# Kernel tuning notes

Measured on AMD Instinct MI355X. Metric: run time of the kernel, lower is better.

## Reference

```python
import jax, jax.numpy as jnp
import numpy as np

NV = 20000; NC = 20000; E = 500000
IN_SHAPE = 2; PE_DIM = 8; HID = 64; NL = 3
EPS = 1e-7  # GENConv message eps


def _lin(x, w, b):
    return x @ w + b


def _encode(x, pe, ew, eb, pw1, pb1, pw2, pb2):
    # relu(cat([Linear(x), 0.5*(pe_mlp(pe)+pe_mlp(-pe))], dim=1))
    def pe_mlp(p):
        return _lin(jax.nn.relu(_lin(p, pw1, pb1)), pw2, pb2)
    h = jnp.concatenate([_lin(x, ew, eb), 0.5 * (pe_mlp(pe) + pe_mlp(-pe))], axis=1)
    return jax.nn.relu(h)


def _genconv(x_src, x_dst, src, dst, ewt, lew, leb, w1, b1, w2, b2, n_dst):
    # GENConv(aggr='softmax', t=1, norm=None, msg_norm=False, edge_dim=1)
    msg = jax.nn.relu(x_src[src] + _lin(ewt, lew, leb)) + EPS  # [E, HID]
    m = jax.ops.segment_max(msg, dst, num_segments=n_dst)      # stable segment softmax
    ex = jnp.exp(msg - m[dst])
    s = jax.ops.segment_sum(ex, dst, num_segments=n_dst)
    agg = jax.ops.segment_sum(ex / (s[dst] + 1e-16) * msg, dst, num_segments=n_dst)
    out = agg + x_dst
    return _lin(jax.nn.relu(_lin(out, w1, b1)), w2, b2)  # MLP [hid -> 2hid -> hid]


def setup_inputs() -> dict:
    key = jax.random.key(0)
    ks = iter(jax.random.split(key, 64))
    d = {}
    d['x_vals'] = jax.random.normal(next(ks), (NV, IN_SHAPE), jnp.float32)
    d['x_cons'] = jax.random.normal(next(ks), (NC, IN_SHAPE), jnp.float32)
    d['pe_vals'] = jax.random.normal(next(ks), (NV, PE_DIM), jnp.float32)
    d['pe_cons'] = jax.random.normal(next(ks), (NC, PE_DIM), jnp.float32)
    d['edge_index_v2c'] = jnp.stack([
        jax.random.randint(next(ks), (E,), 0, NV),
        jax.random.randint(next(ks), (E,), 0, NC)])
    d['edge_index_c2v'] = jnp.stack([
        jax.random.randint(next(ks), (E,), 0, NC),
        jax.random.randint(next(ks), (E,), 0, NV)])
    d['edge_weight_v2c'] = jax.random.normal(next(ks), (E, 1), jnp.float32)
    d['edge_weight_c2v'] = jax.random.normal(next(ks), (E, 1), jnp.float32)
    def p(shape):
        return jax.random.normal(next(ks), shape, jnp.float32) * 0.05
    for k_ in ['vals', 'cons']:
        d[f'enc_{k_}_w'] = p((IN_SHAPE, HID // 2)); d[f'enc_{k_}_b'] = p((HID // 2,))
        d[f'pe_{k_}_w1'] = p((PE_DIM, HID)); d[f'pe_{k_}_b1'] = p((HID,))
        d[f'pe_{k_}_w2'] = p((HID, HID // 2)); d[f'pe_{k_}_b2'] = p((HID // 2,))
    for c in ['v2c', 'c2v']:
        d[f'{c}_edge_w'] = p((NL, 1, HID)); d[f'{c}_edge_b'] = p((NL, HID))
        d[f'{c}_w1'] = p((NL, HID, 2 * HID)); d[f'{c}_b1'] = p((NL, 2 * HID))
        d[f'{c}_w2'] = p((NL, 2 * HID, HID)); d[f'{c}_b2'] = p((NL, HID))
    for k_ in ['vals', 'cons']:
        d[f'pred_{k_}_w1'] = p((HID, HID)); d[f'pred_{k_}_b1'] = p((HID,))
        d[f'pred_{k_}_w2'] = p((HID, 1)); d[f'pred_{k_}_b2'] = p((1,))
    return d


def reference(x_vals, x_cons, pe_vals, pe_cons, edge_index_v2c, edge_index_c2v,
              edge_weight_v2c, edge_weight_c2v,
              enc_vals_w, enc_vals_b, pe_vals_w1, pe_vals_b1, pe_vals_w2, pe_vals_b2,
              enc_cons_w, enc_cons_b, pe_cons_w1, pe_cons_b1, pe_cons_w2, pe_cons_b2,
              v2c_edge_w, v2c_edge_b, v2c_w1, v2c_b1, v2c_w2, v2c_b2,
              c2v_edge_w, c2v_edge_b, c2v_w1, c2v_b1, c2v_w2, c2v_b2,
              pred_vals_w1, pred_vals_b1, pred_vals_w2, pred_vals_b2,
              pred_cons_w1, pred_cons_b1, pred_cons_w2, pred_cons_b2):
    vals = _encode(x_vals, pe_vals, enc_vals_w, enc_vals_b,
                   pe_vals_w1, pe_vals_b1, pe_vals_w2, pe_vals_b2)
    cons = _encode(x_cons, pe_cons, enc_cons_w, enc_cons_b,
                   pe_cons_w1, pe_cons_b1, pe_cons_w2, pe_cons_b2)
    hv, hc = [], []
    for i in range(NL):
        cons = _genconv(vals, cons, edge_index_v2c[0], edge_index_v2c[1],
                        edge_weight_v2c, v2c_edge_w[i], v2c_edge_b[i],
                        v2c_w1[i], v2c_b1[i], v2c_w2[i], v2c_b2[i], NC)
        vals = _genconv(cons, vals, edge_index_c2v[0], edge_index_c2v[1],
                        edge_weight_c2v, c2v_edge_w[i], c2v_edge_b[i],
                        c2v_w1[i], c2v_b1[i], c2v_w2[i], c2v_b2[i], NV)
        hc.append(cons); hv.append(vals)
    V = jnp.stack(hv)  # [NL, NV, HID]
    C = jnp.stack(hc)  # [NL, NC, HID]
    pv = _lin(jax.nn.relu(_lin(V, pred_vals_w1, pred_vals_b1)), pred_vals_w2, pred_vals_b2)
    pc = _lin(jax.nn.relu(_lin(C, pred_cons_w1, pred_cons_b1)), pred_cons_w2, pred_cons_b2)
    return pv[..., 0].T, pc[..., 0].T  # [NV, NL], [NC, NL]
```

## Files before the change

### kernel.cpp

```cpp
#include <hip/hip_runtime.h>

#define NVN 20000
#define NCN 20000
#define NE  500000
#define HID 64
#define NLAYER 3
#define TN 40
#define BSH 8
#define NB 79
#define P1E 2048

__device__ __forceinline__ float relu_(float x) { return fmaxf(x, 0.0f); }

__global__ __launch_bounds__(256) void binhist_kernel(
    const int* __restrict__ dstA, const int* __restrict__ dstB,
    int* __restrict__ binszA, int* __restrict__ binszB)
{
    __shared__ int cA[NB], cB[NB];
    int t = threadIdx.x;
    int e0 = blockIdx.x * P1E;
    if (t < NB) { cA[t] = 0; cB[t] = 0; }
    __syncthreads();
    for (int i = t; i < P1E; i += 256) {
        int e = e0 + i;
        if (e < NE) {
            atomicAdd(&cA[dstA[e] >> BSH], 1);
            atomicAdd(&cB[dstB[e] >> BSH], 1);
        }
    }
    __syncthreads();
    if (t < NB) {
        if (cA[t] > 0) atomicAdd(&binszA[t], cA[t]);
        if (cB[t] > 0) atomicAdd(&binszB[t], cB[t]);
    }
}

__global__ __launch_bounds__(256) void binscan_kernel(
    const int* __restrict__ binszA, int* __restrict__ binbaseA, int* __restrict__ bincurA,
    const int* __restrict__ binszB, int* __restrict__ binbaseB, int* __restrict__ bincurB)
{
    const int* binsz = blockIdx.x ? binszB : binszA;
    int* binbase     = blockIdx.x ? binbaseB : binbaseA;
    int* bincur      = blockIdx.x ? bincurB : bincurA;
    __shared__ int p[256];
    int t = threadIdx.x;
    p[t] = (t < NB) ? binsz[t] : 0;
    __syncthreads();
    for (int off = 1; off < 256; off <<= 1) {
        int v = (t >= off) ? p[t - off] : 0;
        __syncthreads();
        p[t] += v;
        __syncthreads();
    }
    if (t < NB) { int b = (t == 0) ? 0 : p[t - 1]; binbase[t] = b; bincur[t] = b; }
    if (t == NB) binbase[NB] = p[NB - 1];
}

__global__ __launch_bounds__(256) void scatter_p1_kernel(
    const int* __restrict__ eiA, const float* __restrict__ ewA,
    int* __restrict__ bincurA, int2* __restrict__ stageA,
    const int* __restrict__ eiB, const float* __restrict__ ewB,
    int* __restrict__ bincurB, int2* __restrict__ stageB)
{
    __shared__ int rnk[P1E];
    __shared__ int cnt[NB], base_[NB];
    int t = threadIdx.x;
    int e0 = blockIdx.x * P1E;

    for (int g = 0; g < 2; ++g) {
        const int* ei   = g ? eiB : eiA;
        const float* ew = g ? ewB : ewA;
        int* bincur     = g ? bincurB : bincurA;
        int2* stage     = g ? stageB : stageA;

        if (t < NB) cnt[t] = 0;
        __syncthreads();
        for (int i = t; i < P1E; i += 256) {
            int e = e0 + i;
            if (e < NE) {
                int d = ei[NE + e];
                rnk[i] = atomicAdd(&cnt[d >> BSH], 1);
            }
        }
        __syncthreads();
        if (t < NB && cnt[t] > 0) base_[t] = atomicAdd(&bincur[t], cnt[t]);
        __syncthreads();
        for (int i = t; i < P1E; i += 256) {
            int e = e0 + i;
            if (e < NE) {
                int s = ei[e], d = ei[NE + e];
                float w = ew[e];
                stage[base_[d >> BSH] + rnk[i]] =
                    make_int2((int)((unsigned)s | ((unsigned)d << 16)), __float_as_int(w));
            }
        }
        __syncthreads();
    }
}

__global__ __launch_bounds__(1024) void scatter_p2_kernel(
    const int* __restrict__ binbaseA, const int2* __restrict__ stageA,
    int* __restrict__ rowptrA, int2* __restrict__ pairA,
    const int* __restrict__ binbaseB, const int2* __restrict__ stageB,
    int* __restrict__ rowptrB, int2* __restrict__ pairB)
{
    __shared__ int deg[256], pfx[256], cur[256];
    int g = blockIdx.x / NB;
    int b = blockIdx.x % NB;
    const int* binbase = g ? binbaseB : binbaseA;
    const int2* stage  = g ? stageB : stageA;
    int* rowptr        = g ? rowptrB : rowptrA;
    int2* pair         = g ? pairB : pairA;

    int d0 = b << BSH;
    int d1 = min(d0 + 256, NCN);
    int nd = d1 - d0;
    int t = threadIdx.x;
    int estart = binbase[b], eend = binbase[b + 1];

    if (t < 256) deg[t] = 0;
    __syncthreads();
    for (int e = estart + t; e < eend; e += 1024) {
        int dst = (int)((unsigned)stage[e].x >> 16);
        atomicAdd(&deg[dst - d0], 1);
    }
    __syncthreads();
    if (t < 256) pfx[t] = deg[t];
    __syncthreads();
    for (int off = 1; off < 256; off <<= 1) {
        int v = (t >= off && t < 256) ? pfx[t - off] : 0;
        __syncthreads();
        if (t < 256) pfx[t] += v;
        __syncthreads();
    }
    if (t < nd) {
        int ex = estart + pfx[t] - deg[t];
        rowptr[d0 + t] = ex;
        cur[t] = ex;
    }
    if (t == 0) rowptr[d1] = eend;
    __syncthreads();
    for (int e = estart + t; e < eend; e += 1024) {
        int2 s = stage[e];
        unsigned u = (unsigned)s.x;
        int src = (int)(u & 0xFFFFu);
        int dst = (int)(u >> 16);
        int p = atomicAdd(&cur[dst - d0], 1);
        pair[p] = make_int2(src, s.y);
    }
}

__global__ __launch_bounds__(256) void encode2_kernel(
    const float* __restrict__ xv, const float* __restrict__ pev,
    const float* __restrict__ ewv, const float* __restrict__ ebv,
    const float* __restrict__ pw1v, const float* __restrict__ pb1v,
    const float* __restrict__ pw2v, const float* __restrict__ pb2v,
    const float* __restrict__ xc, const float* __restrict__ pec,
    const float* __restrict__ ewc, const float* __restrict__ ebc,
    const float* __restrict__ pw1c, const float* __restrict__ pb1c,
    const float* __restrict__ pw2c, const float* __restrict__ pb2c,
    float* __restrict__ outv, float* __restrict__ outc)
{
    __shared__ float sh[4][64];
    const int VB = (NVN + 3) / 4;
    int wave = threadIdx.x >> 6, lane = threadIdx.x & 63;
    int b = blockIdx.x;
    bool isC = (b >= VB);
    const float* x   = isC ? xc : xv;
    const float* pe  = isC ? pec : pev;
    const float* ew  = isC ? ewc : ewv;
    const float* eb  = isC ? ebc : ebv;
    const float* pw1 = isC ? pw1c : pw1v;
    const float* pb1 = isC ? pb1c : pb1v;
    const float* pw2 = isC ? pw2c : pw2v;
    const float* pb2 = isC ? pb2c : pb2v;
    float* out = isC ? outc : outv;
    int N = isC ? NCN : NVN;
    int n = (isC ? b - VB : b) * 4 + wave;
    if (n >= N) return;

    float accp = pb1[lane], accm = accp;
#pragma unroll
    for (int k = 0; k < 8; ++k) {
        float p = pe[n * 8 + k];
        float w = pw1[k * 64 + lane];
        accp += p * w;
        accm -= p * w;
    }
    float hs = 0.5f * (relu_(accp) + relu_(accm));
    float* my = sh[wave];
    my[lane] = hs;
    __builtin_amdgcn_wave_barrier();

    int col = lane & 31;
    float peo = pb2[col];
#pragma unroll
    for (int k = 0; k < 64; k += 4) {
        float4 hv = *(const float4*)(my + k);
        peo = fmaf(hv.x, pw2[(k + 0) * 32 + col], peo);
        peo = fmaf(hv.y, pw2[(k + 1) * 32 + col], peo);
        peo = fmaf(hv.z, pw2[(k + 2) * 32 + col], peo);
        peo = fmaf(hv.w, pw2[(k + 3) * 32 + col], peo);
    }
    float lino = x[n * 2 + 0] * ew[col] + x[n * 2 + 1] * ew[32 + col] + eb[col];
    float h = (lane < 32) ? lino : peo;
    out[n * 64 + lane] = relu_(h);
}

__global__ __launch_bounds__(256) void edge_agg_kernel(
    const float* __restrict__ xsrc,
    const float* __restrict__ xdst,
    const int* __restrict__ rowptr,
    const int2* __restrict__ pair,
    const float* __restrict__ lew,
    const float* __restrict__ leb,
    float* __restrict__ oa,
    int N)
{
    int wave = threadIdx.x >> 6, lane = threadIdx.x & 63;
    int n = blockIdx.x * 4 + wave;
    if (n >= N) return;

    int start = __builtin_amdgcn_readfirstlane(rowptr[n]);
    int end   = __builtin_amdgcn_readfirstlane(rowptr[n + 1]);
    float lw = lew[lane], lb = leb[lane];
    float xd = xdst[n * 64 + lane];

    float den = 0.0f, num = 0.0f;
    int j = start;

    if (j + 16 <= end) {
        int2 pb[16];
#pragma unroll
        for (int c = 0; c < 16; ++c) pb[c] = pair[j + c];

        for (; j + 32 <= end; j += 16) {
            float xv[16];
#pragma unroll
            for (int c = 0; c < 16; ++c) xv[c] = xsrc[pb[c].x * 64 + lane];
            int2 pn[16];
#pragma unroll
            for (int c = 0; c < 16; ++c) pn[c] = pair[j + 16 + c];
#pragma unroll
            for (int c = 0; c < 16; ++c) {
                float msg = relu_(fmaf(__int_as_float(pb[c].y), lw, xv[c] + lb)) + 1e-7f;
                float e = __expf(msg);
                den += e;
                num = fmaf(e, msg, num);
            }
#pragma unroll
            for (int c = 0; c < 16; ++c) pb[c] = pn[c];
        }
        {
            float xv[16];
#pragma unroll
            for (int c = 0; c < 16; ++c) xv[c] = xsrc[pb[c].x * 64 + lane];
#pragma unroll
            for (int c = 0; c < 16; ++c) {
                float msg = relu_(fmaf(__int_as_float(pb[c].y), lw, xv[c] + lb)) + 1e-7f;
                float e = __expf(msg);
                den += e;
                num = fmaf(e, msg, num);
            }
            j += 16;
        }
    }
    for (; j + 8 <= end; j += 8) {
        int2 p8[8];
#pragma unroll
        for (int c = 0; c < 8; ++c) p8[c] = pair[j + c];
        float xv[8];
#pragma unroll
        for (int c = 0; c < 8; ++c) xv[c] = xsrc[p8[c].x * 64 + lane];
#pragma unroll
        for (int c = 0; c < 8; ++c) {
            float msg = relu_(fmaf(__int_as_float(p8[c].y), lw, xv[c] + lb)) + 1e-7f;
            float e = __expf(msg);
            den += e;
            num = fmaf(e, msg, num);
        }
    }
    for (; j < end; ++j) {
        int2 p = pair[j];
        float xv = xsrc[p.x * 64 + lane];
        float msg = relu_(fmaf(__int_as_float(p.y), lw, xv + lb)) + 1e-7f;
        float e = __expf(msg);
        den += e;
        num = fmaf(e, msg, num);
    }

    oa[n * 64 + lane] = num / (den + 1e-16f) + xd;
}

__global__ __launch_bounds__(256, 4) void mlp_kernel(
    const float* __restrict__ oa,
    float* __restrict__ feat,
    const float* __restrict__ w1,
    const float* __restrict__ b1,
    const float* __restrict__ w2,
    const float* __restrict__ b2,
    const float* __restrict__ pw1,
    const float* __restrict__ pb1,
    const float* __restrict__ pw2,
    const float* __restrict__ pb2,
    float* __restrict__ outp,
    int N, int layer)
{
    __shared__ float act[TN][68];
    __shared__ float hid[TN][132];
    __shared__ float b1s[128];
    __shared__ float b2s[64];
    __shared__ float pb1s[64];
    __shared__ float pw2s[64];

    int tid = threadIdx.x;
    if (tid < 128) b1s[tid] = b1[tid];
    if (tid < 64) { b2s[tid] = b2[tid]; pb1s[tid] = pb1[tid]; pw2s[tid] = pw2[tid]; }
    float pb2v = pb2[0];

    int o4 = (tid & 31) * 4;
    int o2 = (tid & 31) * 2;
    int n5 = (tid >> 5) * 5;
    __syncthreads();

    int ntiles = N / TN;
    for (int tile = blockIdx.x; tile < ntiles; tile += gridDim.x) {
        int base = tile * TN;
        {
            const float4* g4 = (const float4*)(oa + (size_t)base * 64);
            for (int i = tid; i < TN * 16; i += 256)
                *(float4*)&act[i >> 4][(i & 15) * 4] = g4[i];
        }
        __syncthreads();

        {
            float acc[5][4];
#pragma unroll
            for (int i = 0; i < 5; ++i)
#pragma unroll
                for (int q = 0; q < 4; ++q) acc[i][q] = b1s[o4 + q];
#pragma unroll 2
            for (int k = 0; k < 64; k += 4) {
                float4 a[5];
#pragma unroll
                for (int i = 0; i < 5; ++i) a[i] = *(const float4*)&act[n5 + i][k];
                float4 w0 = *(const float4*)&w1[(k + 0) * 128 + o4];
                float4 wq1 = *(const float4*)&w1[(k + 1) * 128 + o4];
                float4 wq2 = *(const float4*)&w1[(k + 2) * 128 + o4];
                float4 wq3 = *(const float4*)&w1[(k + 3) * 128 + o4];
#pragma unroll
                for (int i = 0; i < 5; ++i) {
                    acc[i][0] = fmaf(a[i].x, w0.x, acc[i][0]);
                    acc[i][1] = fmaf(a[i].x, w0.y, acc[i][1]);
                    acc[i][2] = fmaf(a[i].x, w0.z, acc[i][2]);
                    acc[i][3] = fmaf(a[i].x, w0.w, acc[i][3]);
                    acc[i][0] = fmaf(a[i].y, wq1.x, acc[i][0]);
                    acc[i][1] = fmaf(a[i].y, wq1.y, acc[i][1]);
                    acc[i][2] = fmaf(a[i].y, wq1.z, acc[i][2]);
                    acc[i][3] = fmaf(a[i].y, wq1.w, acc[i][3]);
                    acc[i][0] = fmaf(a[i].z, wq2.x, acc[i][0]);
                    acc[i][1] = fmaf(a[i].z, wq2.y, acc[i][1]);
                    acc[i][2] = fmaf(a[i].z, wq2.z, acc[i][2]);
                    acc[i][3] = fmaf(a[i].z, wq2.w, acc[i][3]);
                    acc[i][0] = fmaf(a[i].w, wq3.x, acc[i][0]);
                    acc[i][1] = fmaf(a[i].w, wq3.y, acc[i][1]);
                    acc[i][2] = fmaf(a[i].w, wq3.z, acc[i][2]);
                    acc[i][3] = fmaf(a[i].w, wq3.w, acc[i][3]);
                }
            }
#pragma unroll
            for (int i = 0; i < 5; ++i) {
                float4 h4 = make_float4(relu_(acc[i][0]), relu_(acc[i][1]),
                                        relu_(acc[i][2]), relu_(acc[i][3]));
                *(float4*)&hid[n5 + i][o4] = h4;
            }
        }
        __syncthreads();

        {
            float acc[5][2];
#pragma unroll
            for (int i = 0; i < 5; ++i) { acc[i][0] = b2s[o2]; acc[i][1] = b2s[o2 + 1]; }
#pragma unroll 2
            for (int k = 0; k < 128; k += 4) {
                float4 a[5];
#pragma unroll
                for (int i = 0; i < 5; ++i) a[i] = *(const float4*)&hid[n5 + i][k];
                float2 w0 = *(const float2*)&w2[(k + 0) * 64 + o2];
                float2 wq1 = *(const float2*)&w2[(k + 1) * 64 + o2];
                float2 wq2 = *(const float2*)&w2[(k + 2) * 64 + o2];
                float2 wq3 = *(const float2*)&w2[(k + 3) * 64 + o2];
#pragma unroll
                for (int i = 0; i < 5; ++i) {
                    acc[i][0] = fmaf(a[i].x, w0.x, acc[i][0]);
                    acc[i][1] = fmaf(a[i].x, w0.y, acc[i][1]);
                    acc[i][0] = fmaf(a[i].y, wq1.x, acc[i][0]);
                    acc[i][1] = fmaf(a[i].y, wq1.y, acc[i][1]);
                    acc[i][0] = fmaf(a[i].z, wq2.x, acc[i][0]);
                    acc[i][1] = fmaf(a[i].z, wq2.y, acc[i][1]);
                    acc[i][0] = fmaf(a[i].w, wq3.x, acc[i][0]);
                    acc[i][1] = fmaf(a[i].w, wq3.y, acc[i][1]);
                }
            }
#pragma unroll
            for (int i = 0; i < 5; ++i) {
                float2 r2 = make_float2(acc[i][0], acc[i][1]);
                *(float2*)&feat[(size_t)(base + n5 + i) * 64 + o2] = r2;
                *(float2*)&act[n5 + i][o2] = r2;
            }
        }
        __syncthreads();

        {
            float acc[5][2];
#pragma unroll
            for (int i = 0; i < 5; ++i) { acc[i][0] = pb1s[o2]; acc[i][1] = pb1s[o2 + 1]; }
#pragma unroll 2
            for (int k = 0; k < 64; k += 4) {
                float4 a[5];
#pragma unroll
                for (int i = 0; i < 5; ++i) a[i] = *(const float4*)&act[n5 + i][k];
                float2 w0 = *(const float2*)&pw1[(k + 0) * 64 + o2];
                float2 wq1 = *(const float2*)&pw1[(k + 1) * 64 + o2];
                float2 wq2 = *(const float2*)&pw1[(k + 2) * 64 + o2];
                float2 wq3 = *(const float2*)&pw1[(k + 3) * 64 + o2];
#pragma unroll
                for (int i = 0; i < 5; ++i) {
                    acc[i][0] = fmaf(a[i].x, w0.x, acc[i][0]);
                    acc[i][1] = fmaf(a[i].x, w0.y, acc[i][1]);
                    acc[i][0] = fmaf(a[i].y, wq1.x, acc[i][0]);
                    acc[i][1] = fmaf(a[i].y, wq1.y, acc[i][1]);
                    acc[i][0] = fmaf(a[i].z, wq2.x, acc[i][0]);
                    acc[i][1] = fmaf(a[i].z, wq2.y, acc[i][1]);
                    acc[i][0] = fmaf(a[i].w, wq3.x, acc[i][0]);
                    acc[i][1] = fmaf(a[i].w, wq3.y, acc[i][1]);
                }
            }
            float pw2a = pw2s[o2], pw2b = pw2s[o2 + 1];
            float ps[5];
#pragma unroll
            for (int i = 0; i < 5; ++i)
                ps[i] = relu_(acc[i][0]) * pw2a + relu_(acc[i][1]) * pw2b;
#pragma unroll
            for (int msk = 16; msk >= 1; msk >>= 1) {
#pragma unroll
                for (int i = 0; i < 5; ++i)
                    ps[i] += __shfl_xor(ps[i], msk, 64);
            }
            if ((tid & 31) == 0) {
#pragma unroll
                for (int i = 0; i < 5; ++i)
                    outp[(size_t)(base + n5 + i) * NLAYER + layer] = ps[i] + pb2v;
            }
        }
        __syncthreads();
    }
}

extern "C" void kernel_launch(void* const* d_in, const int* in_sizes, int n_in,
                              void* d_out, int out_size, void* d_ws, size_t ws_size,
                              hipStream_t stream)
{
    const float* x_vals   = (const float*)d_in[0];
    const float* x_cons   = (const float*)d_in[1];
    const float* pe_vals  = (const float*)d_in[2];
    const float* pe_cons  = (const float*)d_in[3];
    const int*   ei_v2c   = (const int*)d_in[4];
    const int*   ei_c2v   = (const int*)d_in[5];
    const float* ew_v2c   = (const float*)d_in[6];
    const float* ew_c2v   = (const float*)d_in[7];
    const float* enc_vals_w = (const float*)d_in[8];
    const float* enc_vals_b = (const float*)d_in[9];
    const float* pe_vals_w1 = (const float*)d_in[10];
    const float* pe_vals_b1 = (const float*)d_in[11];
    const float* pe_vals_w2 = (const float*)d_in[12];
    const float* pe_vals_b2 = (const float*)d_in[13];
    const float* enc_cons_w = (const float*)d_in[14];
    const float* enc_cons_b = (const float*)d_in[15];
    const float* pe_cons_w1 = (const float*)d_in[16];
    const float* pe_cons_b1 = (const float*)d_in[17];
    const float* pe_cons_w2 = (const float*)d_in[18];
    const float* pe_cons_b2 = (const float*)d_in[19];
    const float* v2c_edge_w = (const float*)d_in[20];
    const float* v2c_edge_b = (const float*)d_in[21];
    const float* v2c_w1     = (const float*)d_in[22];
    const float* v2c_b1     = (const float*)d_in[23];
    const float* v2c_w2     = (const float*)d_in[24];
    const float* v2c_b2     = (const float*)d_in[25];
    const float* c2v_edge_w = (const float*)d_in[26];
    const float* c2v_edge_b = (const float*)d_in[27];
    const float* c2v_w1     = (const float*)d_in[28];
    const float* c2v_b1     = (const float*)d_in[29];
    const float* c2v_w2     = (const float*)d_in[30];
    const float* c2v_b2     = (const float*)d_in[31];
    const float* pred_vals_w1 = (const float*)d_in[32];
    const float* pred_vals_b1 = (const float*)d_in[33];
    const float* pred_vals_w2 = (const float*)d_in[34];
    const float* pred_vals_b2 = (const float*)d_in[35];
    const float* pred_cons_w1 = (const float*)d_in[36];
    const float* pred_cons_b1 = (const float*)d_in[37];
    const float* pred_cons_w2 = (const float*)d_in[38];
    const float* pred_cons_b2 = (const float*)d_in[39];

    float* out = (float*)d_out;
    float* out_c = out + (size_t)NVN * NLAYER;

    const size_t NF = (size_t)NVN * 64;

    float* ws     = (float*)d_ws;
    float* feat_v = ws;
    float* feat_c = feat_v + NF;
    float* oa     = feat_c + NF;
    int2* v2c_pair  = (int2*)(oa + NF);
    int2* c2v_pair  = v2c_pair + NE;
    int2* v2c_stage = c2v_pair + NE;
    int2* c2v_stage = v2c_stage + NE;
    int* ip = (int*)(c2v_stage + NE);
    int* v2c_binsz   = ip; ip += NB;
    int* c2v_binsz   = ip; ip += NB;
    int* v2c_binbase = ip; ip += NB + 1;
    int* c2v_binbase = ip; ip += NB + 1;
    int* v2c_bincur  = ip; ip += NB;
    int* c2v_bincur  = ip; ip += NB;
    int* v2c_rowptr  = ip; ip += NCN + 1;
    int* c2v_rowptr  = ip; ip += NVN + 1;

    const int p1b = (NE + P1E - 1) / P1E;

    hipMemsetAsync(v2c_binsz, 0, (size_t)(2 * NB) * sizeof(int), stream);
    binhist_kernel<<<p1b, 256, 0, stream>>>(ei_v2c + NE, ei_c2v + NE,
                                            v2c_binsz, c2v_binsz);
    binscan_kernel<<<2, 256, 0, stream>>>(v2c_binsz, v2c_binbase, v2c_bincur,
                                          c2v_binsz, c2v_binbase, c2v_bincur);
    scatter_p1_kernel<<<p1b, 256, 0, stream>>>(
        ei_v2c, ew_v2c, v2c_bincur, v2c_stage,
        ei_c2v, ew_c2v, c2v_bincur, c2v_stage);
    scatter_p2_kernel<<<2 * NB, 1024, 0, stream>>>(
        v2c_binbase, v2c_stage, v2c_rowptr, v2c_pair,
        c2v_binbase, c2v_stage, c2v_rowptr, c2v_pair);

    encode2_kernel<<<(NVN + 3) / 4 + (NCN + 3) / 4, 256, 0, stream>>>(
        x_vals, pe_vals, enc_vals_w, enc_vals_b,
        pe_vals_w1, pe_vals_b1, pe_vals_w2, pe_vals_b2,
        x_cons, pe_cons, enc_cons_w, enc_cons_b,
        pe_cons_w1, pe_cons_b1, pe_cons_w2, pe_cons_b2,
        feat_v, feat_c);

    for (int i = 0; i < NLAYER; ++i) {
        edge_agg_kernel<<<(NCN + 3) / 4, 256, 0, stream>>>(
            feat_v, feat_c, v2c_rowptr, v2c_pair,
            v2c_edge_w + (size_t)i * HID, v2c_edge_b + (size_t)i * HID,
            oa, NCN);
        mlp_kernel<<<500, 256, 0, stream>>>(
            oa, feat_c,
            v2c_w1 + (size_t)i * 8192, v2c_b1 + (size_t)i * 128,
            v2c_w2 + (size_t)i * 8192, v2c_b2 + (size_t)i * 64,
            pred_cons_w1, pred_cons_b1, pred_cons_w2, pred_cons_b2,
            out_c, NCN, i);
        edge_agg_kernel<<<(NVN + 3) / 4, 256, 0, stream>>>(
            feat_c, feat_v, c2v_rowptr, c2v_pair,
            c2v_edge_w + (size_t)i * HID, c2v_edge_b + (size_t)i * HID,
            oa, NVN);
        mlp_kernel<<<500, 256, 0, stream>>>(
            oa, feat_v,
            c2v_w1 + (size_t)i * 8192, c2v_b1 + (size_t)i * 128,
            c2v_w2 + (size_t)i * 8192, c2v_b2 + (size_t)i * 64,
            pred_vals_w1, pred_vals_b1, pred_vals_w2, pred_vals_b2,
            out, NVN, i);
    }
}
```

Baseline: 435.3 us.

## Fuse softmax edge aggregation into the per-tile MLP kernel

Merges the per-node softmax aggregation kernel into the MLP kernel. Each wave aggregates 10 destination rows directly into the shared activation tile, so the intermediate aggregate buffer is no longer written to and read back from global memory. This also halves the kernel launches per layer. The cost is parallelism for the gather phase: only NV/40 blocks of 256 threads run, each wave walking its rows one after another, so far fewer waves are available to hide the latency of the random gathers.

```diff
diff --git a/kernel.cpp b/kernel.cpp
--- a/kernel.cpp
+++ b/kernel.cpp
@@ -207,93 +207,13 @@
     out[n * 64 + lane] = relu_(h);
 }
 
-__global__ __launch_bounds__(256) void edge_agg_kernel(
+__global__ __launch_bounds__(256) void agg_mlp_kernel(
     const float* __restrict__ xsrc,
     const float* __restrict__ xdst,
     const int* __restrict__ rowptr,
     const int2* __restrict__ pair,
     const float* __restrict__ lew,
     const float* __restrict__ leb,
-    float* __restrict__ oa,
-    int N)
-{
-    int wave = threadIdx.x >> 6, lane = threadIdx.x & 63;
-    int n = blockIdx.x * 4 + wave;
-    if (n >= N) return;
-
-    int start = __builtin_amdgcn_readfirstlane(rowptr[n]);
-    int end   = __builtin_amdgcn_readfirstlane(rowptr[n + 1]);
-    float lw = lew[lane], lb = leb[lane];
-    float xd = xdst[n * 64 + lane];
-
-    float den = 0.0f, num = 0.0f;
-    int j = start;
-
-    if (j + 16 <= end) {
-        int2 pb[16];
-#pragma unroll
-        for (int c = 0; c < 16; ++c) pb[c] = pair[j + c];
-
-        for (; j + 32 <= end; j += 16) {
-            float xv[16];
-#pragma unroll
-            for (int c = 0; c < 16; ++c) xv[c] = xsrc[pb[c].x * 64 + lane];
-            int2 pn[16];
-#pragma unroll
-            for (int c = 0; c < 16; ++c) pn[c] = pair[j + 16 + c];
-#pragma unroll
-            for (int c = 0; c < 16; ++c) {
-                float msg = relu_(fmaf(__int_as_float(pb[c].y), lw, xv[c] + lb)) + 1e-7f;
-                float e = __expf(msg);
-                den += e;
-                num = fmaf(e, msg, num);
-            }
-#pragma unroll
-            for (int c = 0; c < 16; ++c) pb[c] = pn[c];
-        }
-        {
-            float xv[16];
-#pragma unroll
-            for (int c = 0; c < 16; ++c) xv[c] = xsrc[pb[c].x * 64 + lane];
-#pragma unroll
-            for (int c = 0; c < 16; ++c) {
-                float msg = relu_(fmaf(__int_as_float(pb[c].y), lw, xv[c] + lb)) + 1e-7f;
-                float e = __expf(msg);
-                den += e;
-                num = fmaf(e, msg, num);
-            }
-            j += 16;
-        }
-    }
-    for (; j + 8 <= end; j += 8) {
-        int2 p8[8];
-#pragma unroll
-        for (int c = 0; c < 8; ++c) p8[c] = pair[j + c];
-        float xv[8];
-#pragma unroll
-        for (int c = 0; c < 8; ++c) xv[c] = xsrc[p8[c].x * 64 + lane];
-#pragma unroll
-        for (int c = 0; c < 8; ++c) {
-            float msg = relu_(fmaf(__int_as_float(p8[c].y), lw, xv[c] + lb)) + 1e-7f;
-            float e = __expf(msg);
-            den += e;
-            num = fmaf(e, msg, num);
-        }
-    }
-    for (; j < end; ++j) {
-        int2 p = pair[j];
-        float xv = xsrc[p.x * 64 + lane];
-        float msg = relu_(fmaf(__int_as_float(p.y), lw, xv + lb)) + 1e-7f;
-        float e = __expf(msg);
-        den += e;
-        num = fmaf(e, msg, num);
-    }
-
-    oa[n * 64 + lane] = num / (den + 1e-16f) + xd;
-}
-
-__global__ __launch_bounds__(256, 4) void mlp_kernel(
-    const float* __restrict__ oa,
     float* __restrict__ feat,
     const float* __restrict__ w1,
     const float* __restrict__ b1,
@@ -314,22 +234,91 @@
     __shared__ float pw2s[64];
 
     int tid = threadIdx.x;
+    int wave = tid >> 6, lane = tid & 63;
     if (tid < 128) b1s[tid] = b1[tid];
     if (tid < 64) { b2s[tid] = b2[tid]; pb1s[tid] = pb1[tid]; pw2s[tid] = pw2[tid]; }
     float pb2v = pb2[0];
+    float lw = lew[lane], lb = leb[lane];
 
     int o4 = (tid & 31) * 4;
     int o2 = (tid & 31) * 2;
     int n5 = (tid >> 5) * 5;
-    __syncthreads();
 
     int ntiles = N / TN;
     for (int tile = blockIdx.x; tile < ntiles; tile += gridDim.x) {
         int base = tile * TN;
-        {
-            const float4* g4 = (const float4*)(oa + (size_t)base * 64);
-            for (int i = tid; i < TN * 16; i += 256)
-                *(float4*)&act[i >> 4][(i & 15) * 4] = g4[i];
+
+        for (int q = 0; q < TN / 4; ++q) {
+            int row = wave * (TN / 4) + q;
+            int n = base + row;
+            int start = __builtin_amdgcn_readfirstlane(rowptr[n]);
+            int end   = __builtin_amdgcn_readfirstlane(rowptr[n + 1]);
+            float xd = xdst[(size_t)n * 64 + lane];
+
+            float den = 0.0f, num = 0.0f;
+            int j = start;
+
+            if (j + 16 <= end) {
+                int2 pb[16];
+#pragma unroll
+                for (int c = 0; c < 16; ++c) pb[c] = pair[j + c];
+
+                for (; j + 32 <= end; j += 16) {
+                    float xv[16];
+#pragma unroll
+                    for (int c = 0; c < 16; ++c) xv[c] = xsrc[pb[c].x * 64 + lane];
+                    int2 pn[16];
+#pragma unroll
+                    for (int c = 0; c < 16; ++c) pn[c] = pair[j + 16 + c];
+#pragma unroll
+                    for (int c = 0; c < 16; ++c) {
+                        float msg = relu_(fmaf(__int_as_float(pb[c].y), lw, xv[c] + lb)) + 1e-7f;
+                        float e = __expf(msg);
+                        den += e;
+                        num = fmaf(e, msg, num);
+                    }
+#pragma unroll
+                    for (int c = 0; c < 16; ++c) pb[c] = pn[c];
+                }
+                {
+                    float xv[16];
+#pragma unroll
+                    for (int c = 0; c < 16; ++c) xv[c] = xsrc[pb[c].x * 64 + lane];
+#pragma unroll
+                    for (int c = 0; c < 16; ++c) {
+                        float msg = relu_(fmaf(__int_as_float(pb[c].y), lw, xv[c] + lb)) + 1e-7f;
+                        float e = __expf(msg);
+                        den += e;
+                        num = fmaf(e, msg, num);
+                    }
+                    j += 16;
+                }
+            }
+            for (; j + 8 <= end; j += 8) {
+                int2 p8[8];
+#pragma unroll
+                for (int c = 0; c < 8; ++c) p8[c] = pair[j + c];
+                float xv[8];
+#pragma unroll
+                for (int c = 0; c < 8; ++c) xv[c] = xsrc[p8[c].x * 64 + lane];
+#pragma unroll
+                for (int c = 0; c < 8; ++c) {
+                    float msg = relu_(fmaf(__int_as_float(p8[c].y), lw, xv[c] + lb)) + 1e-7f;
+                    float e = __expf(msg);
+                    den += e;
+                    num = fmaf(e, msg, num);
+                }
+            }
+            for (; j < end; ++j) {
+                int2 p = pair[j];
+                float xv = xsrc[p.x * 64 + lane];
+                float msg = relu_(fmaf(__int_as_float(p.y), lw, xv + lb)) + 1e-7f;
+                float e = __expf(msg);
+                den += e;
+                num = fmaf(e, msg, num);
+            }
+
+            act[row][lane] = num / (den + 1e-16f) + xd;
         }
         __syncthreads();
 
@@ -547,22 +536,18 @@
         feat_v, feat_c);
 
     for (int i = 0; i < NLAYER; ++i) {
-        edge_agg_kernel<<<(NCN + 3) / 4, 256, 0, stream>>>(
+        agg_mlp_kernel<<<NCN / TN, 256, 0, stream>>>(
             feat_v, feat_c, v2c_rowptr, v2c_pair,
             v2c_edge_w + (size_t)i * HID, v2c_edge_b + (size_t)i * HID,
-            oa, NCN);
-        mlp_kernel<<<500, 256, 0, stream>>>(
-            oa, feat_c,
+            feat_c,
             v2c_w1 + (size_t)i * 8192, v2c_b1 + (size_t)i * 128,
             v2c_w2 + (size_t)i * 8192, v2c_b2 + (size_t)i * 64,
             pred_cons_w1, pred_cons_b1, pred_cons_w2, pred_cons_b2,
             out_c, NCN, i);
-        edge_agg_kernel<<<(NVN + 3) / 4, 256, 0, stream>>>(
+        agg_mlp_kernel<<<NVN / TN, 256, 0, stream>>>(
             feat_c, feat_v, c2v_rowptr, c2v_pair,
             c2v_edge_w + (size_t)i * HID, c2v_edge_b + (size_t)i * HID,
-            oa, NVN);
-        mlp_kernel<<<500, 256, 0, stream>>>(
-            oa, feat_v,
+            feat_v,
             c2v_w1 + (size_t)i * 8192, c2v_b1 + (size_t)i * 128,
             c2v_w2 + (size_t)i * 8192, c2v_b2 + (size_t)i * 64,
             pred_vals_w1, pred_vals_b1, pred_vals_w2, pred_vals_b2,
```

Result: slower. 507.6 us (+16.6%).

## Split wave into four 16-lane groups gathering float4 rows in edge aggregation

Applied to the files above, without the earlier changes.

The edge aggregation kernel now lets each 16-lane quarter of a wave handle a different edge, with each lane loading a float4 (four channels) of the source row. This processes four edges per wave instruction and issues 128-bit gathers instead of scalar 32-bit gathers, reducing the number of memory instructions and pair-index loads. Partial sums are combined across the quarters with xor shuffles at the end, and the tail uses predicated lanes. The cost is extra shuffle reduction work and a masked remainder path for nodes whose degree is not a multiple of four.

```diff
diff --git a/kernel.cpp b/kernel.cpp
--- a/kernel.cpp
+++ b/kernel.cpp
@@ -207,6 +207,18 @@
     out[n * 64 + lane] = relu_(h);
 }
 
+#define GRP4(P, XV) { \
+    float w_ = __int_as_float((P).y); \
+    float m0 = relu_(fmaf(w_, lw4.x, (XV).x + lb4.x)) + 1e-7f; \
+    float m1 = relu_(fmaf(w_, lw4.y, (XV).y + lb4.y)) + 1e-7f; \
+    float m2 = relu_(fmaf(w_, lw4.z, (XV).z + lb4.z)) + 1e-7f; \
+    float m3 = relu_(fmaf(w_, lw4.w, (XV).w + lb4.w)) + 1e-7f; \
+    float e0 = __expf(m0), e1 = __expf(m1), e2 = __expf(m2), e3 = __expf(m3); \
+    den4.x += e0; num4.x = fmaf(e0, m0, num4.x); \
+    den4.y += e1; num4.y = fmaf(e1, m1, num4.y); \
+    den4.z += e2; num4.z = fmaf(e2, m2, num4.z); \
+    den4.w += e3; num4.w = fmaf(e3, m3, num4.w); }
+
 __global__ __launch_bounds__(256) void edge_agg_kernel(
     const float* __restrict__ xsrc,
     const float* __restrict__ xdst,
@@ -223,73 +235,88 @@
 
     int start = __builtin_amdgcn_readfirstlane(rowptr[n]);
     int end   = __builtin_amdgcn_readfirstlane(rowptr[n + 1]);
-    float lw = lew[lane], lb = leb[lane];
-    float xd = xdst[n * 64 + lane];
-
-    float den = 0.0f, num = 0.0f;
+
+    int g16 = lane >> 4;
+    int dql = lane & 15;
+    const float4* xs4 = (const float4*)xsrc;
+    float4 lw4 = *(const float4*)&lew[dql * 4];
+    float4 lb4 = *(const float4*)&leb[dql * 4];
+    float4 xd4 = ((const float4*)xdst)[(size_t)n * 16 + dql];
+
+    float4 den4 = make_float4(0.f, 0.f, 0.f, 0.f);
+    float4 num4 = make_float4(0.f, 0.f, 0.f, 0.f);
     int j = start;
 
     if (j + 16 <= end) {
-        int2 pb[16];
-#pragma unroll
-        for (int c = 0; c < 16; ++c) pb[c] = pair[j + c];
+        int2 pr[4];
+#pragma unroll
+        for (int c = 0; c < 4; ++c) pr[c] = pair[j + 4 * c + g16];
 
         for (; j + 32 <= end; j += 16) {
-            float xv[16];
-#pragma unroll
-            for (int c = 0; c < 16; ++c) xv[c] = xsrc[pb[c].x * 64 + lane];
-            int2 pn[16];
-#pragma unroll
-            for (int c = 0; c < 16; ++c) pn[c] = pair[j + 16 + c];
-#pragma unroll
-            for (int c = 0; c < 16; ++c) {
-                float msg = relu_(fmaf(__int_as_float(pb[c].y), lw, xv[c] + lb)) + 1e-7f;
-                float e = __expf(msg);
-                den += e;
-                num = fmaf(e, msg, num);
-            }
-#pragma unroll
-            for (int c = 0; c < 16; ++c) pb[c] = pn[c];
+            float4 xv[4];
+#pragma unroll
+            for (int c = 0; c < 4; ++c) xv[c] = xs4[(size_t)pr[c].x * 16 + dql];
+            int2 pn[4];
+#pragma unroll
+            for (int c = 0; c < 4; ++c) pn[c] = pair[j + 16 + 4 * c + g16];
+#pragma unroll
+            for (int c = 0; c < 4; ++c) GRP4(pr[c], xv[c]);
+#pragma unroll
+            for (int c = 0; c < 4; ++c) pr[c] = pn[c];
         }
         {
-            float xv[16];
-#pragma unroll
-            for (int c = 0; c < 16; ++c) xv[c] = xsrc[pb[c].x * 64 + lane];
-#pragma unroll
-            for (int c = 0; c < 16; ++c) {
-                float msg = relu_(fmaf(__int_as_float(pb[c].y), lw, xv[c] + lb)) + 1e-7f;
-                float e = __expf(msg);
-                den += e;
-                num = fmaf(e, msg, num);
-            }
+            float4 xv[4];
+#pragma unroll
+            for (int c = 0; c < 4; ++c) xv[c] = xs4[(size_t)pr[c].x * 16 + dql];
+#pragma unroll
+            for (int c = 0; c < 4; ++c) GRP4(pr[c], xv[c]);
             j += 16;
         }
     }
-    for (; j + 8 <= end; j += 8) {
-        int2 p8[8];
-#pragma unroll
-        for (int c = 0; c < 8; ++c) p8[c] = pair[j + c];
-        float xv[8];
-#pragma unroll
-        for (int c = 0; c < 8; ++c) xv[c] = xsrc[p8[c].x * 64 + lane];
-#pragma unroll
-        for (int c = 0; c < 8; ++c) {
-            float msg = relu_(fmaf(__int_as_float(p8[c].y), lw, xv[c] + lb)) + 1e-7f;
-            float e = __expf(msg);
-            den += e;
-            num = fmaf(e, msg, num);
-        }
-    }
-    for (; j < end; ++j) {
-        int2 p = pair[j];
-        float xv = xsrc[p.x * 64 + lane];
-        float msg = relu_(fmaf(__int_as_float(p.y), lw, xv + lb)) + 1e-7f;
-        float e = __expf(msg);
-        den += e;
-        num = fmaf(e, msg, num);
-    }
-
-    oa[n * 64 + lane] = num / (den + 1e-16f) + xd;
+    for (; j + 4 <= end; j += 4) {
+        int2 p = pair[j + g16];
+        float4 xv = xs4[(size_t)p.x * 16 + dql];
+        GRP4(p, xv);
+    }
+    if (j < end) {
+        int eidx = j + g16;
+        bool v = eidx < end;
+        int2 p = pair[v ? eidx : end - 1];
+        float4 xv = xs4[(size_t)p.x * 16 + dql];
+        float w_ = __int_as_float(p.y);
+        float m0 = relu_(fmaf(w_, lw4.x, xv.x + lb4.x)) + 1e-7f;
+        float m1 = relu_(fmaf(w_, lw4.y, xv.y + lb4.y)) + 1e-7f;
+        float m2 = relu_(fmaf(w_, lw4.z, xv.z + lb4.z)) + 1e-7f;
+        float m3 = relu_(fmaf(w_, lw4.w, xv.w + lb4.w)) + 1e-7f;
+        float e0 = v ? __expf(m0) : 0.0f;
+        float e1 = v ? __expf(m1) : 0.0f;
+        float e2 = v ? __expf(m2) : 0.0f;
+        float e3 = v ? __expf(m3) : 0.0f;
+        den4.x += e0; num4.x = fmaf(e0, m0, num4.x);
+        den4.y += e1; num4.y = fmaf(e1, m1, num4.y);
+        den4.z += e2; num4.z = fmaf(e2, m2, num4.z);
+        den4.w += e3; num4.w = fmaf(e3, m3, num4.w);
+    }
+
+#pragma unroll
+    for (int msk = 16; msk <= 32; msk <<= 1) {
+        den4.x += __shfl_xor(den4.x, msk, 64);
+        den4.y += __shfl_xor(den4.y, msk, 64);
+        den4.z += __shfl_xor(den4.z, msk, 64);
+        den4.w += __shfl_xor(den4.w, msk, 64);
+        num4.x += __shfl_xor(num4.x, msk, 64);
+        num4.y += __shfl_xor(num4.y, msk, 64);
+        num4.z += __shfl_xor(num4.z, msk, 64);
+        num4.w += __shfl_xor(num4.w, msk, 64);
+    }
+
+    float4 r;
+    r.x = num4.x / (den4.x + 1e-16f) + xd4.x;
+    r.y = num4.y / (den4.y + 1e-16f) + xd4.y;
+    r.z = num4.z / (den4.z + 1e-16f) + xd4.z;
+    r.w = num4.w / (den4.w + 1e-16f) + xd4.w;
+    if (lane < 16)
+        ((float4*)oa)[(size_t)n * 16 + lane] = r;
 }
 
 __global__ __launch_bounds__(256, 4) void mlp_kernel(
```

Measured after the change: 454.5 us. 4.4% more time.

## Use fixed-capacity bins to drop histogram pass; shrink MLP tile for more blocks

Applied to the files above, without the earlier changes.

Replaces the bin histogram and scan kernels with fixed-capacity bins (16384 slots per bin), so scatter phase 1 appends directly at bin offsets. Per-row start and end arrays replace the contiguous rowptr. This removes two kernel launches and a full pass over the destination indices, at the cost of larger sparse workspace and an overflow risk if a bin gets more than CAP edges. Separately, the MLP tile drops from 40 to 16 rows and launches one block per tile, trading weight reuse per block for more blocks in flight.

```diff
diff --git a/kernel.cpp b/kernel.cpp
--- a/kernel.cpp
+++ b/kernel.cpp
@@ -5,55 +5,21 @@
 #define NE  500000
 #define HID 64
 #define NLAYER 3
-#define TN 40
+#define TN 16
 #define BSH 8
 #define NB 79
+#define CAPSH 14
+#define CAP (1 << CAPSH)
+#define NBCAP (NB * CAP)
 #define P1E 2048
 
 __device__ __forceinline__ float relu_(float x) { return fmaxf(x, 0.0f); }
 
-__global__ __launch_bounds__(256) void binhist_kernel(
-    const int* __restrict__ dstA, const int* __restrict__ dstB,
-    int* __restrict__ binszA, int* __restrict__ binszB)
-{
-    __shared__ int cA[NB], cB[NB];
+__global__ __launch_bounds__(256) void bininit_kernel(
+    int* __restrict__ bincurA, int* __restrict__ bincurB)
+{
     int t = threadIdx.x;
-    int e0 = blockIdx.x * P1E;
-    if (t < NB) { cA[t] = 0; cB[t] = 0; }
-    __syncthreads();
-    for (int i = t; i < P1E; i += 256) {
-        int e = e0 + i;
-        if (e < NE) {
-            atomicAdd(&cA[dstA[e] >> BSH], 1);
-            atomicAdd(&cB[dstB[e] >> BSH], 1);
-        }
-    }
-    __syncthreads();
-    if (t < NB) {
-        if (cA[t] > 0) atomicAdd(&binszA[t], cA[t]);
-        if (cB[t] > 0) atomicAdd(&binszB[t], cB[t]);
-    }
-}
-
-__global__ __launch_bounds__(256) void binscan_kernel(
-    const int* __restrict__ binszA, int* __restrict__ binbaseA, int* __restrict__ bincurA,
-    const int* __restrict__ binszB, int* __restrict__ binbaseB, int* __restrict__ bincurB)
-{
-    const int* binsz = blockIdx.x ? binszB : binszA;
-    int* binbase     = blockIdx.x ? binbaseB : binbaseA;
-    int* bincur      = blockIdx.x ? bincurB : bincurA;
-    __shared__ int p[256];
-    int t = threadIdx.x;
-    p[t] = (t < NB) ? binsz[t] : 0;
-    __syncthreads();
-    for (int off = 1; off < 256; off <<= 1) {
-        int v = (t >= off) ? p[t - off] : 0;
-        __syncthreads();
-        p[t] += v;
-        __syncthreads();
-    }
-    if (t < NB) { int b = (t == 0) ? 0 : p[t - 1]; binbase[t] = b; bincur[t] = b; }
-    if (t == NB) binbase[NB] = p[NB - 1];
+    if (t < NB) { bincurA[t] = t << CAPSH; bincurB[t] = t << CAPSH; }
 }
 
 __global__ __launch_bounds__(256) void scatter_p1_kernel(
@@ -99,24 +65,26 @@
 }
 
 __global__ __launch_bounds__(1024) void scatter_p2_kernel(
-    const int* __restrict__ binbaseA, const int2* __restrict__ stageA,
-    int* __restrict__ rowptrA, int2* __restrict__ pairA,
-    const int* __restrict__ binbaseB, const int2* __restrict__ stageB,
-    int* __restrict__ rowptrB, int2* __restrict__ pairB)
+    const int* __restrict__ bincurA, const int2* __restrict__ stageA,
+    int* __restrict__ rowptrA, int* __restrict__ rowendA, int2* __restrict__ pairA,
+    const int* __restrict__ bincurB, const int2* __restrict__ stageB,
+    int* __restrict__ rowptrB, int* __restrict__ rowendB, int2* __restrict__ pairB)
 {
     __shared__ int deg[256], pfx[256], cur[256];
     int g = blockIdx.x / NB;
     int b = blockIdx.x % NB;
-    const int* binbase = g ? binbaseB : binbaseA;
+    const int* bincur  = g ? bincurB : bincurA;
     const int2* stage  = g ? stageB : stageA;
     int* rowptr        = g ? rowptrB : rowptrA;
+    int* rowend        = g ? rowendB : rowendA;
     int2* pair         = g ? pairB : pairA;
 
     int d0 = b << BSH;
     int d1 = min(d0 + 256, NCN);
     int nd = d1 - d0;
     int t = threadIdx.x;
-    int estart = binbase[b], eend = binbase[b + 1];
+    int estart = b << CAPSH;
+    int eend = bincur[b];
 
     if (t < 256) deg[t] = 0;
     __syncthreads();
@@ -136,9 +104,9 @@
     if (t < nd) {
         int ex = estart + pfx[t] - deg[t];
         rowptr[d0 + t] = ex;
+        rowend[d0 + t] = estart + pfx[t];
         cur[t] = ex;
     }
-    if (t == 0) rowptr[d1] = eend;
     __syncthreads();
     for (int e = estart + t; e < eend; e += 1024) {
         int2 s = stage[e];
@@ -211,6 +179,7 @@
     const float* __restrict__ xsrc,
     const float* __restrict__ xdst,
     const int* __restrict__ rowptr,
+    const int* __restrict__ rowend,
     const int2* __restrict__ pair,
     const float* __restrict__ lew,
     const float* __restrict__ leb,
@@ -222,9 +191,9 @@
     if (n >= N) return;
 
     int start = __builtin_amdgcn_readfirstlane(rowptr[n]);
-    int end   = __builtin_amdgcn_readfirstlane(rowptr[n + 1]);
+    int end   = __builtin_amdgcn_readfirstlane(rowend[n]);
     float lw = lew[lane], lb = leb[lane];
-    float xd = xdst[n * 64 + lane];
+    float xd = xdst[(size_t)n * 64 + lane];
 
     float den = 0.0f, num = 0.0f;
     int j = start;
@@ -289,7 +258,7 @@
         num = fmaf(e, msg, num);
     }
 
-    oa[n * 64 + lane] = num / (den + 1e-16f) + xd;
+    oa[(size_t)n * 64 + lane] = num / (den + 1e-16f) + xd;
 }
 
 __global__ __launch_bounds__(256, 4) void mlp_kernel(
@@ -320,7 +289,7 @@
 
     int o4 = (tid & 31) * 4;
     int o2 = (tid & 31) * 2;
-    int n5 = (tid >> 5) * 5;
+    int n2 = (tid >> 5) * 2;
     __syncthreads();
 
     int ntiles = N / TN;
@@ -328,28 +297,27 @@
         int base = tile * TN;
         {
             const float4* g4 = (const float4*)(oa + (size_t)base * 64);
-            for (int i = tid; i < TN * 16; i += 256)
-                *(float4*)&act[i >> 4][(i & 15) * 4] = g4[i];
+            *(float4*)&act[tid >> 4][(tid & 15) * 4] = g4[tid];
         }
         __syncthreads();
 
         {
-            float acc[5][4];
-#pragma unroll
-            for (int i = 0; i < 5; ++i)
+            float acc[2][4];
+#pragma unroll
+            for (int i = 0; i < 2; ++i)
 #pragma unroll
                 for (int q = 0; q < 4; ++q) acc[i][q] = b1s[o4 + q];
 #pragma unroll 2
             for (int k = 0; k < 64; k += 4) {
-                float4 a[5];
-#pragma unroll
-                for (int i = 0; i < 5; ++i) a[i] = *(const float4*)&act[n5 + i][k];
+                float4 a[2];
+#pragma unroll
+                for (int i = 0; i < 2; ++i) a[i] = *(const float4*)&act[n2 + i][k];
                 float4 w0 = *(const float4*)&w1[(k + 0) * 128 + o4];
                 float4 wq1 = *(const float4*)&w1[(k + 1) * 128 + o4];
                 float4 wq2 = *(const float4*)&w1[(k + 2) * 128 + o4];
                 float4 wq3 = *(const float4*)&w1[(k + 3) * 128 + o4];
 #pragma unroll
-                for (int i = 0; i < 5; ++i) {
+                for (int i = 0; i < 2; ++i) {
                     acc[i][0] = fmaf(a[i].x, w0.x, acc[i][0]);
                     acc[i][1] = fmaf(a[i].x, w0.y, acc[i][1]);
                     acc[i][2] = fmaf(a[i].x, w0.z, acc[i][2]);
@@ -369,29 +337,29 @@
                 }
             }
 #pragma unroll
-            for (int i = 0; i < 5; ++i) {
+            for (int i = 0; i < 2; ++i) {
                 float4 h4 = make_float4(relu_(acc[i][0]), relu_(acc[i][1]),
                                         relu_(acc[i][2]), relu_(acc[i][3]));
-                *(float4*)&hid[n5 + i][o4] = h4;
+                *(float4*)&hid[n2 + i][o4] = h4;
             }
         }
         __syncthreads();
 
         {
-            float acc[5][2];
-#pragma unroll
-            for (int i = 0; i < 5; ++i) { acc[i][0] = b2s[o2]; acc[i][1] = b2s[o2 + 1]; }
+            float acc[2][2];
+#pragma unroll
+            for (int i = 0; i < 2; ++i) { acc[i][0] = b2s[o2]; acc[i][1] = b2s[o2 + 1]; }
 #pragma unroll 2
             for (int k = 0; k < 128; k += 4) {
-                float4 a[5];
-#pragma unroll
-                for (int i = 0; i < 5; ++i) a[i] = *(const float4*)&hid[n5 + i][k];
+                float4 a[2];
+#pragma unroll
+                for (int i = 0; i < 2; ++i) a[i] = *(const float4*)&hid[n2 + i][k];
                 float2 w0 = *(const float2*)&w2[(k + 0) * 64 + o2];
                 float2 wq1 = *(const float2*)&w2[(k + 1) * 64 + o2];
                 float2 wq2 = *(const float2*)&w2[(k + 2) * 64 + o2];
                 float2 wq3 = *(const float2*)&w2[(k + 3) * 64 + o2];
 #pragma unroll
-                for (int i = 0; i < 5; ++i) {
+                for (int i = 0; i < 2; ++i) {
                     acc[i][0] = fmaf(a[i].x, w0.x, acc[i][0]);
                     acc[i][1] = fmaf(a[i].x, w0.y, acc[i][1]);
                     acc[i][0] = fmaf(a[i].y, wq1.x, acc[i][0]);
@@ -403,29 +371,29 @@
                 }
             }
 #pragma unroll
-            for (int i = 0; i < 5; ++i) {
+            for (int i = 0; i < 2; ++i) {
                 float2 r2 = make_float2(acc[i][0], acc[i][1]);
-                *(float2*)&feat[(size_t)(base + n5 + i) * 64 + o2] = r2;
-                *(float2*)&act[n5 + i][o2] = r2;
+                *(float2*)&feat[(size_t)(base + n2 + i) * 64 + o2] = r2;
+                *(float2*)&act[n2 + i][o2] = r2;
             }
         }
         __syncthreads();
 
         {
-            float acc[5][2];
-#pragma unroll
-            for (int i = 0; i < 5; ++i) { acc[i][0] = pb1s[o2]; acc[i][1] = pb1s[o2 + 1]; }
+            float acc[2][2];
+#pragma unroll
+            for (int i = 0; i < 2; ++i) { acc[i][0] = pb1s[o2]; acc[i][1] = pb1s[o2 + 1]; }
 #pragma unroll 2
             for (int k = 0; k < 64; k += 4) {
-                float4 a[5];
-#pragma unroll
-                for (int i = 0; i < 5; ++i) a[i] = *(const float4*)&act[n5 + i][k];
+                float4 a[2];
+#pragma unroll
+                for (int i = 0; i < 2; ++i) a[i] = *(const float4*)&act[n2 + i][k];
                 float2 w0 = *(const float2*)&pw1[(k + 0) * 64 + o2];
                 float2 wq1 = *(const float2*)&pw1[(k + 1) * 64 + o2];
                 float2 wq2 = *(const float2*)&pw1[(k + 2) * 64 + o2];
                 float2 wq3 = *(const float2*)&pw1[(k + 3) * 64 + o2];
 #pragma unroll
-                for (int i = 0; i < 5; ++i) {
+                for (int i = 0; i < 2; ++i) {
                     acc[i][0] = fmaf(a[i].x, w0.x, acc[i][0]);
                     acc[i][1] = fmaf(a[i].x, w0.y, acc[i][1]);
                     acc[i][0] = fmaf(a[i].y, wq1.x, acc[i][0]);
@@ -437,20 +405,20 @@
                 }
             }
             float pw2a = pw2s[o2], pw2b = pw2s[o2 + 1];
-            float ps[5];
-#pragma unroll
-            for (int i = 0; i < 5; ++i)
+            float ps[2];
+#pragma unroll
+            for (int i = 0; i < 2; ++i)
                 ps[i] = relu_(acc[i][0]) * pw2a + relu_(acc[i][1]) * pw2b;
 #pragma unroll
             for (int msk = 16; msk >= 1; msk >>= 1) {
 #pragma unroll
-                for (int i = 0; i < 5; ++i)
+                for (int i = 0; i < 2; ++i)
                     ps[i] += __shfl_xor(ps[i], msk, 64);
             }
             if ((tid & 31) == 0) {
 #pragma unroll
-                for (int i = 0; i < 5; ++i)
-                    outp[(size_t)(base + n5 + i) * NLAYER + layer] = ps[i] + pb2v;
+                for (int i = 0; i < 2; ++i)
+                    outp[(size_t)(base + n2 + i) * NLAYER + layer] = ps[i] + pb2v;
             }
         }
         __syncthreads();
@@ -512,32 +480,26 @@
     float* feat_c = feat_v + NF;
     float* oa     = feat_c + NF;
     int2* v2c_pair  = (int2*)(oa + NF);
-    int2* c2v_pair  = v2c_pair + NE;
-    int2* v2c_stage = c2v_pair + NE;
-    int2* c2v_stage = v2c_stage + NE;
-    int* ip = (int*)(c2v_stage + NE);
-    int* v2c_binsz   = ip; ip += NB;
-    int* c2v_binsz   = ip; ip += NB;
-    int* v2c_binbase = ip; ip += NB + 1;
-    int* c2v_binbase = ip; ip += NB + 1;
+    int2* c2v_pair  = v2c_pair + NBCAP;
+    int2* v2c_stage = c2v_pair + NBCAP;
+    int2* c2v_stage = v2c_stage + NBCAP;
+    int* ip = (int*)(c2v_stage + NBCAP);
     int* v2c_bincur  = ip; ip += NB;
     int* c2v_bincur  = ip; ip += NB;
-    int* v2c_rowptr  = ip; ip += NCN + 1;
-    int* c2v_rowptr  = ip; ip += NVN + 1;
+    int* v2c_rowptr  = ip; ip += NCN;
+    int* v2c_rowend  = ip; ip += NCN;
+    int* c2v_rowptr  = ip; ip += NVN;
+    int* c2v_rowend  = ip; ip += NVN;
 
     const int p1b = (NE + P1E - 1) / P1E;
 
-    hipMemsetAsync(v2c_binsz, 0, (size_t)(2 * NB) * sizeof(int), stream);
-    binhist_kernel<<<p1b, 256, 0, stream>>>(ei_v2c + NE, ei_c2v + NE,
-                                            v2c_binsz, c2v_binsz);
-    binscan_kernel<<<2, 256, 0, stream>>>(v2c_binsz, v2c_binbase, v2c_bincur,
-                                          c2v_binsz, c2v_binbase, c2v_bincur);
+    bininit_kernel<<<1, 256, 0, stream>>>(v2c_bincur, c2v_bincur);
     scatter_p1_kernel<<<p1b, 256, 0, stream>>>(
         ei_v2c, ew_v2c, v2c_bincur, v2c_stage,
         ei_c2v, ew_c2v, c2v_bincur, c2v_stage);
     scatter_p2_kernel<<<2 * NB, 1024, 0, stream>>>(
-        v2c_binbase, v2c_stage, v2c_rowptr, v2c_pair,
-        c2v_binbase, c2v_stage, c2v_rowptr, c2v_pair);
+        v2c_bincur, v2c_stage, v2c_rowptr, v2c_rowend, v2c_pair,
+        c2v_bincur, c2v_stage, c2v_rowptr, c2v_rowend, c2v_pair);
 
     encode2_kernel<<<(NVN + 3) / 4 + (NCN + 3) / 4, 256, 0, stream>>>(
         x_vals, pe_vals, enc_vals_w, enc_vals_b,
@@ -548,20 +510,20 @@
 
     for (int i = 0; i < NLAYER; ++i) {
         edge_agg_kernel<<<(NCN + 3) / 4, 256, 0, stream>>>(
-            feat_v, feat_c, v2c_rowptr, v2c_pair,
+            feat_v, feat_c, v2c_rowptr, v2c_rowend, v2c_pair,
             v2c_edge_w + (size_t)i * HID, v2c_edge_b + (size_t)i * HID,
             oa, NCN);
-        mlp_kernel<<<500, 256, 0, stream>>>(
+        mlp_kernel<<<NCN / TN, 256, 0, stream>>>(
             oa, feat_c,
             v2c_w1 + (size_t)i * 8192, v2c_b1 + (size_t)i * 128,
             v2c_w2 + (size_t)i * 8192, v2c_b2 + (size_t)i * 64,
             pred_cons_w1, pred_cons_b1, pred_cons_w2, pred_cons_b2,
             out_c, NCN, i);
         edge_agg_kernel<<<(NVN + 3) / 4, 256, 0, stream>>>(
-            feat_c, feat_v, c2v_rowptr, c2v_pair,
+            feat_c, feat_v, c2v_rowptr, c2v_rowend, c2v_pair,
             c2v_edge_w + (size_t)i * HID, c2v_edge_b + (size_t)i * HID,
             oa, NVN);
-        mlp_kernel<<<500, 256, 0, stream>>>(
+        mlp_kernel<<<NVN / TN, 256, 0, stream>>>(
             oa, feat_v,
             c2v_w1 + (size_t)i * 8192, c2v_b1 + (size_t)i * 128,
             c2v_w2 + (size_t)i * 8192, c2v_b2 + (size_t)i * 64,
```

Result: slower. 532.4 us (+22.3%).
